# Kernel tuning notes

Measured on AMD Instinct MI355X. Metric: run time of the kernel, lower is better.

Reference implementation:

```python
import jax, jax.numpy as jnp
import numpy as np
from jax import lax

NPOINT = 1024
RADIUS = 0.2
NSAMPLE = 32
BN_EPS = 1e-5


def fps(xyz, npoint):
    """Deterministic farthest point sampling (start index 0). xyz: (B,N,3) -> (B,npoint) int32."""
    B, N, _ = xyz.shape

    def step(carry, _):
        distance, farthest = carry
        centroid = jnp.take_along_axis(xyz, farthest[:, None, None], axis=1)  # (B,1,3)
        d = jnp.sum((xyz - centroid) ** 2, axis=-1)  # (B,N)
        distance = jnp.minimum(distance, d)
        nxt = jnp.argmax(distance, axis=-1).astype(jnp.int32)
        return (distance, nxt), farthest

    init = (jnp.full((B, N), jnp.inf, dtype=xyz.dtype), jnp.zeros((B,), jnp.int32))
    _, idxs = lax.scan(step, init, None, length=npoint)  # (npoint, B)
    return jnp.transpose(idxs)  # (B, npoint)


def ball_query(radius, nsample, xyz, new_xyz):
    """Deterministic ball query: first nsample in-radius indices (sorted), padded with first hit.
    xyz: (B,N,3), new_xyz: (B,S,3) -> (B,S,nsample) int32."""
    B, N, _ = xyz.shape
    # squared distances via GEMM form to avoid (B,S,N,3) intermediate
    sqr = (jnp.sum(new_xyz ** 2, -1)[:, :, None]
           + jnp.sum(xyz ** 2, -1)[:, None, :]
           - 2.0 * jnp.einsum('bsd,bnd->bsn', new_xyz, xyz))  # (B,S,N)
    idx = jnp.where(sqr <= radius ** 2, jnp.arange(N, dtype=jnp.int32), N)
    idx = jnp.sort(idx, axis=-1)[:, :, :nsample]  # (B,S,K)
    first = idx[:, :, :1]
    first = jnp.where(first == N, 0, first)  # no point in radius -> index 0
    return jnp.where(idx == N, first, idx)


def setup_inputs() -> dict:
    key = jax.random.key(0)
    ks = jax.random.split(key, 8)
    B, N, Cin = 16, 4096, 64
    xyz = jax.random.uniform(ks[0], (B, N, 3), dtype=jnp.float32)
    points = jax.random.normal(ks[1], (B, Cin, N), dtype=jnp.float32)
    chans = [Cin + 3, 64, 64, 128]
    d = {"xyz": xyz, "points": points}
    for i in range(3):
        d[f"w{i}"] = jax.random.normal(ks[2 + i], (chans[i + 1], chans[i]), dtype=jnp.float32) / np.float32(np.sqrt(chans[i]))
        d[f"g{i}"] = jnp.ones((chans[i + 1],), dtype=jnp.float32)
        d[f"b{i}"] = jnp.zeros((chans[i + 1],), dtype=jnp.float32)
    return d


def _forward(xyz, points, params):
    B, N, _ = xyz.shape
    idx = fps(xyz, NPOINT)                                     # (B,S)
    new_xyz = jnp.take_along_axis(xyz, idx[:, :, None], axis=1)  # (B,S,3)
    gidx = ball_query(RADIUS, NSAMPLE, xyz, new_xyz)             # (B,S,K)
    gather = jax.vmap(lambda p, i: p[i])
    grouped_xyz = gather(xyz, gidx) - new_xyz[:, :, None, :]     # (B,S,K,3)
    grouped_pts = gather(jnp.transpose(points, (0, 2, 1)), gidx)  # (B,S,K,C)
    feats = jnp.concatenate([grouped_xyz, grouped_pts], axis=-1)  # (B,S,K,3+C)
    for (w, g, b) in params:
        feats = jnp.einsum('oc,bskc->bsko', w, feats)
        mean = jnp.mean(feats, axis=(0, 1, 2))
        var = jnp.var(feats, axis=(0, 1, 2))
        feats = (feats - mean) * (g * lax.rsqrt(var + BN_EPS)) + b  # BatchNorm (batch stats)
        feats = jax.nn.relu(feats)
    feats = jnp.max(feats, axis=2)               # (B,S,Cout) max-pool over neighbors
    return new_xyz, jnp.transpose(feats, (0, 2, 1))  # (B,Cout,S) channel-first like torch


def reference(xyz, points, w0, g0, b0, w1, g1, b1, w2, g2, b2):
    params = [(w0, g0, b0), (w1, g1, b1), (w2, g2, b2)]
    return _forward(xyz, points, params)
```

## Files before the change

kernel.cpp:

```cpp
#include <hip/hip_runtime.h>

#define DI static __device__ __forceinline__

typedef float v2f __attribute__((ext_vector_type(2)));
typedef __attribute__((ext_vector_type(8))) short bf16x8;
typedef __attribute__((ext_vector_type(4))) float f32x4;

DI unsigned short f2bf(float f) {
  unsigned int u = __float_as_uint(f);
  u = (u + 0x7fffu + ((u >> 16) & 1u)) >> 16;
  return (unsigned short)u;
}
DI float bf2f(unsigned short h) { return __uint_as_float(((unsigned int)h) << 16); }

#define DPP_MAXU(v, ctrl)                                                      \
  {                                                                            \
    unsigned o_ = (unsigned)__builtin_amdgcn_update_dpp((int)(v), (int)(v),    \
                                                        (ctrl), 0xf, 0xf, false); \
    (v) = (o_ > (v)) ? o_ : (v);                                               \
  }
#define DPP_MINU(v, ctrl)                                                      \
  {                                                                            \
    unsigned o_ = (unsigned)__builtin_amdgcn_update_dpp((int)(v), (int)(v),    \
                                                        (ctrl), 0xf, 0xf, false); \
    (v) = (o_ < (v)) ? o_ : (v);                                               \
  }

__global__ __launch_bounds__(256) void fps_kernel(const float* __restrict__ xyz,
                                                  float* __restrict__ newxyz) {
  const int b = blockIdx.x;
  const int t = threadIdx.x;
  const int lane = t & 63, wid = t >> 6;
  const float* X = xyz + (size_t)b * 4096 * 3;
  __shared__ float XL[4096 * 3];
  __shared__ int FI[1024];
  __shared__ unsigned long long slot[2][4];
  for (int idx = t; idx < 12288; idx += 256) XL[idx] = X[idx];
  v2f px[8], py[8], pz[8], dist[8];
#pragma unroll
  for (int q = 0; q < 8; ++q) {
    int i0 = t + (q << 9);
    int i1 = i0 + 256;
    px[q] = (v2f){X[i0 * 3 + 0], X[i1 * 3 + 0]};
    py[q] = (v2f){X[i0 * 3 + 1], X[i1 * 3 + 1]};
    pz[q] = (v2f){X[i0 * 3 + 2], X[i1 * 3 + 2]};
    dist[q] = (v2f){3.402823466e38f, 3.402823466e38f};
  }
  __syncthreads();
  float cx = XL[0], cy = XL[1], cz = XL[2];
  int fi = 0;
  for (int s = 0; s < 1024; ++s) {
    if (t == 0) FI[s] = fi;
    float bv = -1.0f;
    unsigned int bi = 0;
    v2f cxv = (v2f){cx, cx}, cyv = (v2f){cy, cy}, czv = (v2f){cz, cz};
#pragma unroll
    for (int q = 0; q < 8; ++q) {
#pragma clang fp contract(off)
      v2f dx = px[q] - cxv;
      v2f dy = py[q] - cyv;
      v2f dz = pz[q] - czv;
      v2f d = (dx * dx + dy * dy) + dz * dz;
#if __has_builtin(__builtin_elementwise_min)
      v2f nd = __builtin_elementwise_min(dist[q], d);
#else
      v2f nd;
      nd.x = fminf(dist[q].x, d.x);
      nd.y = fminf(dist[q].y, d.y);
#endif
      dist[q] = nd;
      float n0 = nd.x, n1 = nd.y;
      bool c0 = (n0 > bv);
      bv = c0 ? n0 : bv;
      bi = c0 ? (unsigned)(t + (q << 9)) : bi;
      bool c1 = (n1 > bv);
      bv = c1 ? n1 : bv;
      bi = c1 ? (unsigned)(t + (q << 9) + 256) : bi;
    }
    unsigned vb = __float_as_uint(bv);
    unsigned m = vb;
    DPP_MAXU(m, 0x111);
    DPP_MAXU(m, 0x112);
    DPP_MAXU(m, 0x114);
    DPP_MAXU(m, 0x118);
    DPP_MAXU(m, 0x142);
    DPP_MAXU(m, 0x143);
    unsigned wmax = (unsigned)__builtin_amdgcn_readlane((int)m, 63);
    unsigned ik = (vb == wmax) ? bi : 0xFFFFFFFFu;
    DPP_MINU(ik, 0x111);
    DPP_MINU(ik, 0x112);
    DPP_MINU(ik, 0x114);
    DPP_MINU(ik, 0x118);
    DPP_MINU(ik, 0x142);
    DPP_MINU(ik, 0x143);
    unsigned widx = (unsigned)__builtin_amdgcn_readlane((int)ik, 63);
    const int p = s & 1;
    if (lane == 0)
      slot[p][wid] = ((unsigned long long)wmax << 32) | (unsigned long long)(~widx);
    __syncthreads();
    unsigned long long k0 = slot[p][0], k1 = slot[p][1];
    unsigned long long k2 = slot[p][2], k3 = slot[p][3];
    unsigned long long m01 = (k0 >= k1) ? k0 : k1;
    unsigned long long m23 = (k2 >= k3) ? k2 : k3;
    unsigned long long win = (m01 >= m23) ? m01 : m23;
    fi = (int)(~(unsigned int)win);
    cx = XL[fi * 3 + 0];
    cy = XL[fi * 3 + 1];
    cz = XL[fi * 3 + 2];
  }
  __syncthreads();
  float* out = newxyz + (size_t)b * 1024 * 3;
  for (int s2 = t; s2 < 1024; s2 += 256) {
    int f = FI[s2];
    out[s2 * 3 + 0] = XL[f * 3 + 0];
    out[s2 * 3 + 1] = XL[f * 3 + 1];
    out[s2 * 3 + 2] = XL[f * 3 + 2];
  }
}

__global__ __launch_bounds__(256) void p0_kernel(const float* __restrict__ points,
                                                 const float* __restrict__ w0,
                                                 float* __restrict__ P0) {
  const int b = blockIdx.x >> 6;
  const int n0 = (blockIdx.x & 63) << 6;
  const int t = threadIdx.x;
  __shared__ float W[64][64];
  for (int idx = t; idx < 4096; idx += 256) {
    int c = idx >> 6, o = idx & 63;
    W[c][o] = w0[o * 67 + 3 + c];
  }
  __syncthreads();
  const int i = t >> 4, j = t & 15;
  const float* Pb = points + (size_t)b * 64 * 4096 + n0 + 4 * i;
  float acc[4][4] = {};
  for (int c = 0; c < 64; ++c) {
    float4 xv = *(const float4*)(Pb + (size_t)c * 4096);
    float4 wv = *(const float4*)&W[c][4 * j];
    float xr[4] = {xv.x, xv.y, xv.z, xv.w};
    float wr[4] = {wv.x, wv.y, wv.z, wv.w};
#pragma unroll
    for (int rr = 0; rr < 4; ++rr)
#pragma unroll
      for (int oi = 0; oi < 4; ++oi) acc[rr][oi] = fmaf(xr[rr], wr[oi], acc[rr][oi]);
  }
#pragma unroll
  for (int rr = 0; rr < 4; ++rr) {
    float4 vv = make_float4(acc[rr][0], acc[rr][1], acc[rr][2], acc[rr][3]);
    *(float4*)(P0 + ((size_t)b * 4096 + n0 + 4 * i + rr) * 64 + 4 * j) = vv;
  }
}

__global__ __launch_bounds__(256) void ballquery_stats0_kernel(
    const float* __restrict__ xyz, const float* __restrict__ newxyz,
    const float* __restrict__ P0, const float* __restrict__ w0,
    int* __restrict__ gidx, float* __restrict__ partials0) {
  const int t = threadIdx.x;
  const int lane = t & 63, w = t >> 6;
  const int gid = blockIdx.x * 4 + w;
  const int b = gid >> 10;
  __shared__ int sel[4][32];
  __shared__ float red[4][128];
  const float* Xb = xyz + (size_t)b * 4096 * 3;
  const float cx = newxyz[(size_t)gid * 3 + 0];
  const float cy = newxyz[(size_t)gid * 3 + 1];
  const float cz = newxyz[(size_t)gid * 3 + 2];
  const float cs = __fadd_rn(__fadd_rn(__fmul_rn(cx, cx), __fmul_rn(cy, cy)), __fmul_rn(cz, cz));
  int cnt = 0, first = 0;
  bool found = false;
  for (int base = 0; base < 4096; base += 64) {
    int i = base + lane;
    float x = Xb[i * 3 + 0], y = Xb[i * 3 + 1], z = Xb[i * 3 + 2];
    float xs = __fadd_rn(__fadd_rn(__fmul_rn(x, x), __fmul_rn(y, y)), __fmul_rn(z, z));
    float dot = fmaf(cz, z, fmaf(cy, y, __fmul_rn(cx, x)));
    float sqr = __fsub_rn(__fadd_rn(cs, xs), __fmul_rn(2.0f, dot));
    bool ok = sqr <= 0.04f;
    unsigned long long mask = __ballot(ok);
    if (!found && mask != 0ull) { first = base + __builtin_ctzll(mask); found = true; }
    int pre = __popcll(mask & ((1ull << lane) - 1ull));
    int pos = cnt + pre;
    if (ok && pos < 32) sel[w][pos] = i;
    cnt += (int)__popcll(mask);
    if (cnt >= 32) break;
  }
  if (cnt < 32) {
    int pad = found ? first : 0;
    for (int p = cnt + lane; p < 32; p += 64) sel[w][p] = pad;
  }
  __syncthreads();
  if (lane < 32) gidx[(size_t)gid * 32 + lane] = sel[w][lane];
  const int c = lane;
  float wx = w0[c * 67 + 0], wy = w0[c * 67 + 1], wz = w0[c * 67 + 2];
  float ssum = 0.f, ssq = 0.f;
  const float* P0b = P0 + (size_t)b * 4096 * 64;
  for (int k = 0; k < 32; ++k) {
    int g = sel[w][k];
    float gx = Xb[g * 3 + 0] - cx, gy = Xb[g * 3 + 1] - cy, gz = Xb[g * 3 + 2] - cz;
    float a0 = fmaf(wx, gx, fmaf(wy, gy, fmaf(wz, gz, P0b[(size_t)g * 64 + c])));
    ssum += a0;
    ssq = fmaf(a0, a0, ssq);
  }
  red[w][c] = ssum;
  red[w][c + 64] = ssq;
  __syncthreads();
  if (t < 128) {
    float acc = red[0][t] + red[1][t] + red[2][t] + red[3][t];
    partials0[(size_t)t * 4096 + blockIdx.x] = acc;
  }
}

__global__ __launch_bounds__(256) void finalize_kernel(
    const float* __restrict__ partials, int C, int nblk,
    const float* __restrict__ gamma, const float* __restrict__ beta,
    float* __restrict__ scale, float* __restrict__ shift) {
  const int c = blockIdx.x, t = threadIdx.x;
  double s1 = 0.0, s2 = 0.0;
  for (int k = t; k < nblk; k += 256) {
    s1 += (double)partials[(size_t)c * nblk + k];
    s2 += (double)partials[(size_t)(C + c) * nblk + k];
  }
  __shared__ double r1[256], r2[256];
  r1[t] = s1;
  r2[t] = s2;
  __syncthreads();
  for (int off = 128; off > 0; off >>= 1) {
    if (t < off) { r1[t] += r1[t + off]; r2[t] += r2[t + off]; }
    __syncthreads();
  }
  if (t == 0) {
    const double M = 524288.0;
    double mean = r1[0] / M;
    double var = r2[0] / M - mean * mean;
    if (var < 0.0) var = 0.0;
    float sc = gamma[c] * (float)(1.0 / sqrt(var + 1e-5));
    scale[c] = sc;
    shift[c] = beta[c] - (float)mean * sc;
  }
}

__global__ __launch_bounds__(256) void p2_kernel(
    const float* __restrict__ xyz, const float* __restrict__ newxyz,
    const float* __restrict__ P0, const int* __restrict__ gidx,
    const float* __restrict__ w0, const float* __restrict__ w1,
    const float* __restrict__ sc0g, const float* __restrict__ sh0g,
    unsigned short* __restrict__ act1, float* __restrict__ partials1) {
  __shared__ unsigned short W1T[64 * 72];
  __shared__ unsigned short A[64 * 72];
  __shared__ unsigned short Cs[64 * 72];
  __shared__ float S1r[4][68], S2r[4][68];
  __shared__ float w0x[64], w0y[64], w0z[64], sc0[64], sh0[64];
  const int t = threadIdx.x;
  const int lane = t & 63, w = t >> 6;
  const int quad = lane >> 4, l15 = lane & 15;
  for (int idx = t; idx < 4096; idx += 256) {
    int o = idx >> 6, c = idx & 63;
    W1T[o * 72 + c] = f2bf(w1[o * 64 + c]);
  }
  if (t < 64) {
    w0x[t] = w0[t * 67 + 0];
    w0y[t] = w0[t * 67 + 1];
    w0z[t] = w0[t * 67 + 2];
    sc0[t] = sc0g[t];
    sh0[t] = sh0g[t];
  }
  __syncthreads();
  const int rl = t >> 2, cq = t & 3;
  float ssum[4] = {}, ssq[4] = {};
  for (int tile = 0; tile < 8; ++tile) {
    const int rowbase = (blockIdx.x * 8 + tile) << 6;
    {
      int r = rowbase + rl;
      int b = r >> 15, s = (r >> 5) & 1023;
      int g = gidx[r];
      const float* Pt = xyz + ((size_t)b * 4096 + g) * 3;
      const float* Ct = newxyz + ((size_t)b * 1024 + s) * 3;
      float dx = Pt[0] - Ct[0], dy = Pt[1] - Ct[1], dz = Pt[2] - Ct[2];
      const float4* p4 = (const float4*)(P0 + ((size_t)b * 4096 + g) * 64 + cq * 16);
      float4 a0 = p4[0], a1 = p4[1], a2 = p4[2], a3 = p4[3];
      float pv[16] = {a0.x, a0.y, a0.z, a0.w, a1.x, a1.y, a1.z, a1.w,
                      a2.x, a2.y, a2.z, a2.w, a3.x, a3.y, a3.z, a3.w};
      unsigned pk[8];
#pragma unroll
      for (int q = 0; q < 8; ++q) {
        int c0 = cq * 16 + 2 * q, c1 = c0 + 1;
        float aa = fmaf(w0x[c0], dx, fmaf(w0y[c0], dy, fmaf(w0z[c0], dz, pv[2 * q])));
        float bb = fmaf(w0x[c1], dx, fmaf(w0y[c1], dy, fmaf(w0z[c1], dz, pv[2 * q + 1])));
        float r0 = fmaxf(0.f, fmaf(aa, sc0[c0], sh0[c0]));
        float r1 = fmaxf(0.f, fmaf(bb, sc0[c1], sh0[c1]));
        pk[q] = (unsigned)f2bf(r0) | ((unsigned)f2bf(r1) << 16);
      }
      uint4* dst = (uint4*)&A[rl * 72 + cq * 16];
      dst[0] = make_uint4(pk[0], pk[1], pk[2], pk[3]);
      dst[1] = make_uint4(pk[4], pk[5], pk[6], pk[7]);
    }
    __syncthreads();
    const unsigned short* Arow = &A[(w * 16 + l15) * 72 + quad * 8];
    bf16x8 a0 = *(const bf16x8*)(Arow);
    bf16x8 a1 = *(const bf16x8*)(Arow + 32);
#pragma unroll
    for (int nt = 0; nt < 4; ++nt) {
      const unsigned short* Brow = &W1T[(nt * 16 + l15) * 72 + quad * 8];
      bf16x8 b0 = *(const bf16x8*)(Brow);
      bf16x8 b1 = *(const bf16x8*)(Brow + 32);
      f32x4 c0 = {0.f, 0.f, 0.f, 0.f};
      c0 = __builtin_amdgcn_mfma_f32_16x16x32_bf16(a0, b0, c0, 0, 0, 0);
      c0 = __builtin_amdgcn_mfma_f32_16x16x32_bf16(a1, b1, c0, 0, 0, 0);
      int o = nt * 16 + l15;
      int rloc = w * 16 + quad * 4;
#pragma unroll
      for (int reg = 0; reg < 4; ++reg) {
        float y = c0[reg];
        ssum[nt] += y;
        ssq[nt] = fmaf(y, y, ssq[nt]);
        Cs[(rloc + reg) * 72 + o] = f2bf(y);
      }
    }
    __syncthreads();
    {
      const uint4* src = (const uint4*)&Cs[rl * 72 + cq * 16];
      uint4 v0 = src[0], v1 = src[1];
      uint4* dst = (uint4*)(act1 + ((size_t)rowbase + rl) * 64 + cq * 16);
      dst[0] = v0;
      dst[1] = v1;
    }
  }
#pragma unroll
  for (int nt = 0; nt < 4; ++nt) {
    float s1 = ssum[nt];
    s1 += __shfl_xor(s1, 16, 64);
    s1 += __shfl_xor(s1, 32, 64);
    float s2 = ssq[nt];
    s2 += __shfl_xor(s2, 16, 64);
    s2 += __shfl_xor(s2, 32, 64);
    if (quad == 0) {
      S1r[w][nt * 16 + l15] = s1;
      S2r[w][nt * 16 + l15] = s2;
    }
  }
  __syncthreads();
  if (t < 64) {
    int o = t;
    float s1 = S1r[0][o] + S1r[1][o] + S1r[2][o] + S1r[3][o];
    float s2 = S2r[0][o] + S2r[1][o] + S2r[2][o] + S2r[3][o];
    partials1[(size_t)o * 1024 + blockIdx.x] = s1;
    partials1[(size_t)(64 + o) * 1024 + blockIdx.x] = s2;
  }
}

__global__ __launch_bounds__(256) void p3_kernel(
    const unsigned short* __restrict__ act1, const float* __restrict__ w2,
    const float* __restrict__ sc1g, const float* __restrict__ sh1g,
    float* __restrict__ partials2, float* __restrict__ gmx,
    float* __restrict__ gmn) {
  __shared__ unsigned short W2T[128 * 72];
  __shared__ unsigned short A[64 * 72];
  __shared__ float Mred[4][132], Nred[4][132];
  __shared__ float S1r[4][132], S2r[4][132];
  __shared__ float sc1[64], sh1[64];
  const int t = threadIdx.x;
  const int lane = t & 63, w = t >> 6;
  const int quad = lane >> 4, l15 = lane & 15;
  for (int idx = t; idx < 8192; idx += 256) {
    int o = idx >> 6, c = idx & 63;
    W2T[o * 72 + c] = f2bf(w2[o * 64 + c]);
  }
  if (t < 64) { sc1[t] = sc1g[t]; sh1[t] = sh1g[t]; }
  __syncthreads();
  const int rl = t >> 2, cq = t & 3;
  float ssum[8] = {}, ssq[8] = {};
  for (int tile = 0; tile < 8; ++tile) {
    const int rowbase = (blockIdx.x * 8 + tile) << 6;
    {
      size_t r = (size_t)rowbase + rl;
      const uint4* pr = (const uint4*)(act1 + r * 64 + cq * 16);
      uint4 aa = pr[0], bb = pr[1];
      unsigned int uu[8] = {aa.x, aa.y, aa.z, aa.w, bb.x, bb.y, bb.z, bb.w};
      unsigned int pk[8];
#pragma unroll
      for (int q = 0; q < 8; ++q) {
        int c = cq * 16 + 2 * q;
        float v0 = bf2f((unsigned short)(uu[q] & 0xffffu));
        float v1 = bf2f((unsigned short)(uu[q] >> 16));
        float r0 = fmaxf(0.f, fmaf(v0, sc1[c], sh1[c]));
        float r1 = fmaxf(0.f, fmaf(v1, sc1[c + 1], sh1[c + 1]));
        pk[q] = (unsigned)f2bf(r0) | ((unsigned)f2bf(r1) << 16);
      }
      uint4* dst = (uint4*)&A[rl * 72 + cq * 16];
      dst[0] = make_uint4(pk[0], pk[1], pk[2], pk[3]);
      dst[1] = make_uint4(pk[4], pk[5], pk[6], pk[7]);
    }
    __syncthreads();
    const unsigned short* Arow = &A[(w * 16 + l15) * 72 + quad * 8];
    bf16x8 a0 = *(const bf16x8*)(Arow);
    bf16x8 a1 = *(const bf16x8*)(Arow + 32);
    f32x4 acc[8];
#pragma unroll
    for (int nt = 0; nt < 8; ++nt) {
      const unsigned short* Brow = &W2T[(nt * 16 + l15) * 72 + quad * 8];
      bf16x8 b0 = *(const bf16x8*)(Brow);
      bf16x8 b1 = *(const bf16x8*)(Brow + 32);
      f32x4 c0 = {0.f, 0.f, 0.f, 0.f};
      c0 = __builtin_amdgcn_mfma_f32_16x16x32_bf16(a0, b0, c0, 0, 0, 0);
      c0 = __builtin_amdgcn_mfma_f32_16x16x32_bf16(a1, b1, c0, 0, 0, 0);
      acc[nt] = c0;
    }
#pragma unroll
    for (int nt = 0; nt < 8; ++nt) {
      float y0 = acc[nt][0], y1 = acc[nt][1], y2 = acc[nt][2], y3 = acc[nt][3];
      ssum[nt] += ((y0 + y1) + (y2 + y3));
      ssq[nt] = fmaf(y0, y0, ssq[nt]);
      ssq[nt] = fmaf(y1, y1, ssq[nt]);
      ssq[nt] = fmaf(y2, y2, ssq[nt]);
      ssq[nt] = fmaf(y3, y3, ssq[nt]);
      float mx = fmaxf(fmaxf(y0, y1), fmaxf(y2, y3));
      float mn = fminf(fminf(y0, y1), fminf(y2, y3));
      mx = fmaxf(mx, __shfl_xor(mx, 16, 64));
      mx = fmaxf(mx, __shfl_xor(mx, 32, 64));
      mn = fminf(mn, __shfl_xor(mn, 16, 64));
      mn = fminf(mn, __shfl_xor(mn, 32, 64));
      if (quad == 0) {
        Mred[w][nt * 16 + l15] = mx;
        Nred[w][nt * 16 + l15] = mn;
      }
    }
    __syncthreads();
    {
      int o = t & 127, g = t >> 7;
      float mx = fmaxf(Mred[2 * g][o], Mred[2 * g + 1][o]);
      float mn = fminf(Nred[2 * g][o], Nred[2 * g + 1][o]);
      int bb2 = rowbase >> 15;
      int ss2 = ((rowbase >> 5) & 1023) + g;
      size_t oidx = ((size_t)bb2 * 1024 + ss2) * 128 + o;
      gmx[oidx] = mx;
      gmn[oidx] = mn;
    }
    __syncthreads();
  }
#pragma unroll
  for (int nt = 0; nt < 8; ++nt) {
    float s1 = ssum[nt];
    s1 += __shfl_xor(s1, 16, 64);
    s1 += __shfl_xor(s1, 32, 64);
    float s2 = ssq[nt];
    s2 += __shfl_xor(s2, 16, 64);
    s2 += __shfl_xor(s2, 32, 64);
    if (quad == 0) {
      S1r[w][nt * 16 + l15] = s1;
      S2r[w][nt * 16 + l15] = s2;
    }
  }
  __syncthreads();
  if (t < 128) {
    int o = t;
    float s1 = S1r[0][o] + S1r[1][o] + S1r[2][o] + S1r[3][o];
    float s2 = S2r[0][o] + S2r[1][o] + S2r[2][o] + S2r[3][o];
    partials2[(size_t)o * 1024 + blockIdx.x] = s1;
    partials2[(size_t)(128 + o) * 1024 + blockIdx.x] = s2;
  }
}

__global__ __launch_bounds__(256) void p4f_kernel(
    const float* __restrict__ gmx, const float* __restrict__ gmn,
    const float* __restrict__ sc2g, const float* __restrict__ sh2g,
    float* __restrict__ feats) {
  __shared__ float MX[16 * 130], MN[16 * 130];
  const int t = threadIdx.x;
  const int bb = blockIdx.x >> 6;
  const int s0 = (blockIdx.x & 63) << 4;
#pragma unroll
  for (int k = 0; k < 8; ++k) {
    int idx = k * 256 + t;
    int s = idx >> 7, o = idx & 127;
    size_t g = ((size_t)bb * 1024 + s0 + s) * 128 + o;
    MX[s * 130 + o] = gmx[g];
    MN[s * 130 + o] = gmn[g];
  }
  __syncthreads();
  const int oo = t >> 1, shf = t & 1;
  const float sc = sc2g[oo], sh = sh2g[oo];
  float* dst = feats + ((size_t)bb * 128 + oo) * 1024 + s0 + shf * 8;
#pragma unroll
  for (int k = 0; k < 8; ++k) {
    int s = shf * 8 + k;
    float v = (sc >= 0.f) ? MX[s * 130 + oo] : MN[s * 130 + oo];
    dst[k] = fmaxf(0.f, fmaf(v, sc, sh));
  }
}

extern "C" void kernel_launch(void* const* d_in, const int* in_sizes, int n_in,
                              void* d_out, int out_size, void* d_ws, size_t ws_size,
                              hipStream_t stream) {
  const float* xyz = (const float*)d_in[0];
  const float* points = (const float*)d_in[1];
  const float* w0 = (const float*)d_in[2];
  const float* g0 = (const float*)d_in[3];
  const float* b0 = (const float*)d_in[4];
  const float* w1 = (const float*)d_in[5];
  const float* g1 = (const float*)d_in[6];
  const float* b1 = (const float*)d_in[7];
  const float* w2 = (const float*)d_in[8];
  const float* g2 = (const float*)d_in[9];
  const float* b2 = (const float*)d_in[10];

  float* out = (float*)d_out;
  float* newxyz = out;
  float* feats = out + 49152;

  char* ws = (char*)d_ws;
  float* P0 = (float*)ws;
  float* gmx = (float*)ws;
  float* gmn = (float*)(ws + (size_t)(8u << 20));
  int* gidx = (int*)(ws + (size_t)(16u << 20));
  unsigned short* act1 = (unsigned short*)(ws + (size_t)(18u << 20));
  float* partials0 = (float*)(ws + (size_t)(82u << 20));
  float* partials1 = (float*)(ws + (size_t)(84u << 20));
  float* partials2 = (float*)(ws + (size_t)(85u << 20));
  float* sc0 = (float*)(ws + (size_t)(86u << 20));
  float* sh0 = sc0 + 128;
  float* sc1 = sc0 + 256;
  float* sh1 = sc0 + 384;
  float* sc2 = sc0 + 512;
  float* sh2 = sc0 + 640;

  fps_kernel<<<16, 256, 0, stream>>>(xyz, newxyz);
  p0_kernel<<<1024, 256, 0, stream>>>(points, w0, P0);
  ballquery_stats0_kernel<<<4096, 256, 0, stream>>>(xyz, newxyz, P0, w0, gidx, partials0);
  finalize_kernel<<<64, 256, 0, stream>>>(partials0, 64, 4096, g0, b0, sc0, sh0);
  p2_kernel<<<1024, 256, 0, stream>>>(xyz, newxyz, P0, gidx, w0, w1, sc0, sh0, act1, partials1);
  finalize_kernel<<<64, 256, 0, stream>>>(partials1, 64, 1024, g1, b1, sc1, sh1);
  p3_kernel<<<1024, 256, 0, stream>>>(act1, w2, sc1, sh1, partials2, gmx, gmn);
  finalize_kernel<<<128, 256, 0, stream>>>(partials2, 128, 1024, g2, b2, sc2, sh2);
  p4f_kernel<<<1024, 256, 0, stream>>>(gmx, gmn, sc2, sh2, feats);
}
```

Baseline: 874.2 us.

## Fuse FPS and P0 GEMM into one launch to overlap independent work

Merges the serial farthest-point-sampling kernel (16 blocks) and the independent points×W0 projection kernel into a single launch. Blocks 0-15 run FPS at raised wave priority and the remaining 1024 blocks compute P0, so the GEMM runs on idle CUs while FPS's long serial loop proceeds. The shared memory becomes a union, so P0 blocks now reserve FPS-sized LDS, which lowers their occupancy. The P0 inner loop is also restructured to preload 16 weight rows into registers per chunk.

Measured after the change: 840.2 us. 1.04x faster.

```diff
diff --git a/kernel.cpp b/kernel.cpp
--- a/kernel.cpp
+++ b/kernel.cpp
@@ -26,16 +26,66 @@
     (v) = (o_ < (v)) ? o_ : (v);                                               \
   }
 
-__global__ __launch_bounds__(256) void fps_kernel(const float* __restrict__ xyz,
-                                                  float* __restrict__ newxyz) {
+__global__ __launch_bounds__(256) void fps_p0_kernel(
+    const float* __restrict__ xyz, float* __restrict__ newxyz,
+    const float* __restrict__ points, const float* __restrict__ w0,
+    float* __restrict__ P0) {
+  __shared__ union {
+    struct {
+      float XL[4096 * 3];
+      int FI[1024];
+      alignas(32) unsigned long long slot[2][4];
+    } f;
+    float W[64][64];
+  } su;
+  const int t = threadIdx.x;
+
+  if (blockIdx.x >= 16) {
+    const int bid = blockIdx.x - 16;
+    const int b = bid >> 6;
+    const int n0 = (bid & 63) << 6;
+    for (int idx = t; idx < 4096; idx += 256) {
+      int c = idx >> 6, o = idx & 63;
+      su.W[c][o] = w0[o * 67 + 3 + c];
+    }
+    __syncthreads();
+    const int i = t >> 4, j = t & 15;
+    const float* Pb = points + (size_t)b * 64 * 4096 + n0 + 4 * i;
+    float acc[4][4] = {};
+    for (int ch = 0; ch < 4; ++ch) {
+      float wr[16][4];
+#pragma unroll
+      for (int cc = 0; cc < 16; ++cc) {
+        float4 wv = *(const float4*)&su.W[ch * 16 + cc][4 * j];
+        wr[cc][0] = wv.x; wr[cc][1] = wv.y; wr[cc][2] = wv.z; wr[cc][3] = wv.w;
+      }
+#pragma unroll
+      for (int cc = 0; cc < 16; ++cc) {
+        int c = ch * 16 + cc;
+        float4 xv = *(const float4*)(Pb + (size_t)c * 4096);
+        float xr[4] = {xv.x, xv.y, xv.z, xv.w};
+#pragma unroll
+        for (int rr = 0; rr < 4; ++rr)
+#pragma unroll
+          for (int oi = 0; oi < 4; ++oi)
+            acc[rr][oi] = fmaf(xr[rr], wr[cc][oi], acc[rr][oi]);
+      }
+    }
+#pragma unroll
+    for (int rr = 0; rr < 4; ++rr) {
+      float4 vv = make_float4(acc[rr][0], acc[rr][1], acc[rr][2], acc[rr][3]);
+      *(float4*)(P0 + ((size_t)b * 4096 + n0 + 4 * i + rr) * 64 + 4 * j) = vv;
+    }
+    return;
+  }
+
+#if __has_builtin(__builtin_amdgcn_s_setprio)
+  __builtin_amdgcn_s_setprio(3);
+#endif
   const int b = blockIdx.x;
-  const int t = threadIdx.x;
   const int lane = t & 63, wid = t >> 6;
   const float* X = xyz + (size_t)b * 4096 * 3;
-  __shared__ float XL[4096 * 3];
-  __shared__ int FI[1024];
-  __shared__ unsigned long long slot[2][4];
-  for (int idx = t; idx < 12288; idx += 256) XL[idx] = X[idx];
+  for (int idx = t; idx < 12288; idx += 256) su.f.XL[idx] = X[idx];
   v2f px[8], py[8], pz[8], dist[8];
 #pragma unroll
   for (int q = 0; q < 8; ++q) {
@@ -47,10 +97,10 @@
     dist[q] = (v2f){3.402823466e38f, 3.402823466e38f};
   }
   __syncthreads();
-  float cx = XL[0], cy = XL[1], cz = XL[2];
+  float cx = su.f.XL[0], cy = su.f.XL[1], cz = su.f.XL[2];
   int fi = 0;
   for (int s = 0; s < 1024; ++s) {
-    if (t == 0) FI[s] = fi;
+    if (t == 0) su.f.FI[s] = fi;
     float bv = -1.0f;
     unsigned int bi = 0;
     v2f cxv = (v2f){cx, cx}, cyv = (v2f){cy, cy}, czv = (v2f){cz, cz};
@@ -96,57 +146,25 @@
     unsigned widx = (unsigned)__builtin_amdgcn_readlane((int)ik, 63);
     const int p = s & 1;
     if (lane == 0)
-      slot[p][wid] = ((unsigned long long)wmax << 32) | (unsigned long long)(~widx);
-    __syncthreads();
-    unsigned long long k0 = slot[p][0], k1 = slot[p][1];
-    unsigned long long k2 = slot[p][2], k3 = slot[p][3];
+      su.f.slot[p][wid] = ((unsigned long long)wmax << 32) | (unsigned long long)(~widx);
+    __syncthreads();
+    unsigned long long k0 = su.f.slot[p][0], k1 = su.f.slot[p][1];
+    unsigned long long k2 = su.f.slot[p][2], k3 = su.f.slot[p][3];
     unsigned long long m01 = (k0 >= k1) ? k0 : k1;
     unsigned long long m23 = (k2 >= k3) ? k2 : k3;
     unsigned long long win = (m01 >= m23) ? m01 : m23;
     fi = (int)(~(unsigned int)win);
-    cx = XL[fi * 3 + 0];
-    cy = XL[fi * 3 + 1];
-    cz = XL[fi * 3 + 2];
+    cx = su.f.XL[fi * 3 + 0];
+    cy = su.f.XL[fi * 3 + 1];
+    cz = su.f.XL[fi * 3 + 2];
   }
   __syncthreads();
   float* out = newxyz + (size_t)b * 1024 * 3;
   for (int s2 = t; s2 < 1024; s2 += 256) {
-    int f = FI[s2];
-    out[s2 * 3 + 0] = XL[f * 3 + 0];
-    out[s2 * 3 + 1] = XL[f * 3 + 1];
-    out[s2 * 3 + 2] = XL[f * 3 + 2];
-  }
-}
-
-__global__ __launch_bounds__(256) void p0_kernel(const float* __restrict__ points,
-                                                 const float* __restrict__ w0,
-                                                 float* __restrict__ P0) {
-  const int b = blockIdx.x >> 6;
-  const int n0 = (blockIdx.x & 63) << 6;
-  const int t = threadIdx.x;
-  __shared__ float W[64][64];
-  for (int idx = t; idx < 4096; idx += 256) {
-    int c = idx >> 6, o = idx & 63;
-    W[c][o] = w0[o * 67 + 3 + c];
-  }
-  __syncthreads();
-  const int i = t >> 4, j = t & 15;
-  const float* Pb = points + (size_t)b * 64 * 4096 + n0 + 4 * i;
-  float acc[4][4] = {};
-  for (int c = 0; c < 64; ++c) {
-    float4 xv = *(const float4*)(Pb + (size_t)c * 4096);
-    float4 wv = *(const float4*)&W[c][4 * j];
-    float xr[4] = {xv.x, xv.y, xv.z, xv.w};
-    float wr[4] = {wv.x, wv.y, wv.z, wv.w};
-#pragma unroll
-    for (int rr = 0; rr < 4; ++rr)
-#pragma unroll
-      for (int oi = 0; oi < 4; ++oi) acc[rr][oi] = fmaf(xr[rr], wr[oi], acc[rr][oi]);
-  }
-#pragma unroll
-  for (int rr = 0; rr < 4; ++rr) {
-    float4 vv = make_float4(acc[rr][0], acc[rr][1], acc[rr][2], acc[rr][3]);
-    *(float4*)(P0 + ((size_t)b * 4096 + n0 + 4 * i + rr) * 64 + 4 * j) = vv;
+    int f = su.f.FI[s2];
+    out[s2 * 3 + 0] = su.f.XL[f * 3 + 0];
+    out[s2 * 3 + 1] = su.f.XL[f * 3 + 1];
+    out[s2 * 3 + 2] = su.f.XL[f * 3 + 2];
   }
 }
 
@@ -521,8 +539,7 @@
   float* sc2 = sc0 + 512;
   float* sh2 = sc0 + 640;
 
-  fps_kernel<<<16, 256, 0, stream>>>(xyz, newxyz);
-  p0_kernel<<<1024, 256, 0, stream>>>(points, w0, P0);
+  fps_p0_kernel<<<1040, 256, 0, stream>>>(xyz, newxyz, points, w0, P0);
   ballquery_stats0_kernel<<<4096, 256, 0, stream>>>(xyz, newxyz, P0, w0, gidx, partials0);
   finalize_kernel<<<64, 256, 0, stream>>>(partials0, 64, 4096, g0, b0, sc0, sh0);
   p2_kernel<<<1024, 256, 0, stream>>>(xyz, newxyz, P0, gidx, w0, w1, sc0, sh0, act1, partials1);
```
